# Kernel optimization log

Measured on AMD Instinct MI355X. Metric: run time of the kernel, lower is better.

The kernel has to match this reference:

```python
import jax, jax.numpy as jnp
import numpy as np

B, T, D, H = 512, 2048, 256, 256  # batch, seq_len, input_size, hidden_size


def _uniform(key, shape, fan_in):
    b = 1.0 / np.sqrt(fan_in)
    return jax.random.uniform(key, shape, minval=-b, maxval=b, dtype=jnp.float32)


def setup_inputs() -> dict:
    key = jax.random.key(0)
    ks = jax.random.split(key, 12)
    return {
        "input_tensor": jax.random.normal(ks[0], (B, T, D), dtype=jnp.float32),
        # fc_i: Linear(D, D)
        "Wi": _uniform(ks[1], (D, D), D), "bi": _uniform(ks[2], (D,), D),
        # fc_h: Linear(H, H)
        "Wh": _uniform(ks[3], (H, H), H), "bh": _uniform(ks[4], (H,), H),
        # fc_a: Linear(D, D)
        "Wa": _uniform(ks[5], (D, D), D), "ba": _uniform(ks[6], (D,), D),
        # LSTM(input_size=D, hidden_size=H), gates ordered [i, f, g, o]
        "W_ih": _uniform(ks[7], (4 * H, D), H), "b_ih": _uniform(ks[8], (4 * H,), H),
        "W_hh": _uniform(ks[9], (4 * H, H), H), "b_hh": _uniform(ks[10], (4 * H,), H),
    }


def reference(input_tensor, Wi, bi, Wh, bh, Wa, ba, W_ih, W_hh, b_ih, b_hh):
    x = input_tensor                      # (B, T, D)
    Bb = x.shape[0]
    Hh = Wh.shape[0]
    h0 = jnp.zeros((Bb, Hh), x.dtype)
    c0 = jnp.zeros((Bb, Hh), x.dtype)

    # Per-timestep FC attention; hidden state never updates in the loop,
    # so it vectorizes exactly over T.
    input_o = jnp.einsum('btd,ed->bte', x, Wi) + bi          # (B, T, D)
    hidden_o = h0 @ Wh.T + bh                                # (B, H) == (B, D)
    pre = input_o + hidden_o[:, None, :]                     # (B, T, D)
    attn = jax.nn.sigmoid(jnp.einsum('btd,ed->bte', pre, Wa) + ba)
    attention_output = jnp.sum(attn * x, axis=1)             # (B, D)

    # LSTM over a length-1 sequence (single cell step), PyTorch gate order i,f,g,o
    gates = attention_output @ W_ih.T + b_ih + h0 @ W_hh.T + b_hh
    i, f, g, o = jnp.split(gates, 4, axis=-1)
    i = jax.nn.sigmoid(i); f = jax.nn.sigmoid(f)
    g = jnp.tanh(g); o = jax.nn.sigmoid(o)
    c = f * c0 + i * g
    h = o * jnp.tanh(c)

    lstm_output = h[None]                                    # (1, B, H)
    return (lstm_output, h[None], c[None])
```

## Files before the change

kernel.cpp:

```cpp
#include <hip/hip_runtime.h>
#include <hip/hip_bf16.h>

typedef _Float16 f16x8 __attribute__((ext_vector_type(8)));
typedef _Float16 f16x4 __attribute__((ext_vector_type(4)));
typedef float    f32x4 __attribute__((ext_vector_type(4)));

#define B_SZ 512
#define T_SZ 2048
#define D_SZ 256
#define TCHUNK 16
#define NCHUNK (T_SZ / TCHUNK)

__global__ __launch_bounds__(256) void prep_kernel(
    const float* __restrict__ Wa, const float* __restrict__ Wi,
    const float* __restrict__ bi, const float* __restrict__ bh,
    const float* __restrict__ ba,
    _Float16* __restrict__ Weff, float* __restrict__ beff)
{
    int e = blockIdx.x;
    int d = threadIdx.x;
    float a0 = 0.f, a1 = 0.f, a2 = 0.f, a3 = 0.f;
    #pragma unroll 4
    for (int k = 0; k < 256; k += 4) {
        a0 = fmaf(Wa[e*256 + k    ], Wi[(k    )*256 + d], a0);
        a1 = fmaf(Wa[e*256 + k + 1], Wi[(k + 1)*256 + d], a1);
        a2 = fmaf(Wa[e*256 + k + 2], Wi[(k + 2)*256 + d], a2);
        a3 = fmaf(Wa[e*256 + k + 3], Wi[(k + 3)*256 + d], a3);
    }
    Weff[e*256 + d] = (_Float16)((a0 + a1) + (a2 + a3));

    __shared__ float red[4];
    float s = Wa[e*256 + d] * (bi[d] + bh[d]);
    s += __shfl_down(s, 32, 64);
    s += __shfl_down(s, 16, 64);
    s += __shfl_down(s,  8, 64);
    s += __shfl_down(s,  4, 64);
    s += __shfl_down(s,  2, 64);
    s += __shfl_down(s,  1, 64);
    if ((d & 63) == 0) red[d >> 6] = s;
    __syncthreads();
    if (d == 0) beff[e] = ba[e] + ((red[0] + red[1]) + (red[2] + red[3]));
}

__global__ __launch_bounds__(512, 4) void attn_kernel(
    const float* __restrict__ x,
    const _Float16* __restrict__ Weff,
    const float* __restrict__ beff,
    float* __restrict__ ao)
{
    const int b    = blockIdx.x;
    const int tid  = threadIdx.x;
    const int wave = tid >> 6;
    const int lane = tid & 63;
    const int l15  = lane & 15;
    const int lq   = lane >> 4;

    __shared__ _Float16 xs[2][TCHUNK * 256];
    char* xsb0 = reinterpret_cast<char*>(&xs[0][0]);
    char* xsb1 = reinterpret_cast<char*>(&xs[1][0]);

    const int col0 = wave*32 + l15;
    const int col1 = col0 + 16;
    f16x8 bfA[8], bfB[8];
    #pragma unroll
    for (int ks = 0; ks < 8; ++ks) {
        bfA[ks] = *reinterpret_cast<const f16x8*>(&Weff[col0*256 + ks*32 + lq*8]);
        bfB[ks] = *reinterpret_cast<const f16x8*>(&Weff[col1*256 + ks*32 + lq*8]);
    }
    const f32x4 bcA = *reinterpret_cast<const f32x4*>(&beff[wave*32 + lq*4]);
    const f32x4 bcB = *reinterpret_cast<const f32x4*>(&beff[wave*32 + 16 + lq*4]);

    const float* xb = x + (size_t)b * T_SZ * D_SZ;

    const int srow = tid >> 5;
    const int scg  = tid & 31;
    const float* srcp = xb + (size_t)srow * 256 + scg * 8;
    const int swb = (srow*512 + scg*16) ^ ((srow & 7) << 4);

    #define LOADC(R, c)                                                            \
        {                                                                          \
            const float* p = srcp + (size_t)(c) * (TCHUNK * D_SZ);                 \
            R##0 = *reinterpret_cast<const f32x4*>(p);                             \
            R##1 = *reinterpret_cast<const f32x4*>(p + 4);                         \
        }

    #define WRITE(BUF, R)                                                          \
        {                                                                          \
            f16x8 h;                                                               \
            h[0] = (_Float16)R##0[0]; h[1] = (_Float16)R##0[1];                    \
            h[2] = (_Float16)R##0[2]; h[3] = (_Float16)R##0[3];                    \
            h[4] = (_Float16)R##1[0]; h[5] = (_Float16)R##1[1];                    \
            h[6] = (_Float16)R##1[2]; h[7] = (_Float16)R##1[3];                    \
            *reinterpret_cast<f16x8*>((BUF) + swb) = h;                            \
        }

    #define SYNC()                                                                 \
        {                                                                          \
            asm volatile("s_waitcnt lgkmcnt(0)" ::: "memory");                     \
            __builtin_amdgcn_sched_barrier(0);                                     \
            __builtin_amdgcn_s_barrier();                                          \
        }

    #define COMPUTE(BUF)                                                           \
        {                                                                          \
            const int aswz  = (l15 & 7) << 4;                                      \
            const int abase = l15 * 512;                                           \
            f32x4 acc0 = {0.f, 0.f, 0.f, 0.f};                                     \
            f32x4 acc1 = {0.f, 0.f, 0.f, 0.f};                                     \
            _Pragma("unroll")                                                      \
            for (int ks = 0; ks < 8; ++ks) {                                       \
                int ab = abase + ((ks*64 + lq*16) ^ aswz);                         \
                f16x8 a = *reinterpret_cast<const f16x8*>((BUF) + ab);             \
                acc0 = __builtin_amdgcn_mfma_f32_16x16x32_f16(bfA[ks], a, acc0, 0, 0, 0); \
                acc1 = __builtin_amdgcn_mfma_f32_16x16x32_f16(bfB[ks], a, acc1, 0, 0, 0); \
            }                                                                      \
             \
            int eb0 = abase + (((wave*64      ) + lq*8) ^ aswz);                   \
            int eb1 = abase + (((wave*64 + 32 ) + lq*8) ^ aswz);                   \
            f16x4 xq0 = *reinterpret_cast<const f16x4*>((BUF) + eb0);              \
            f16x4 xq1 = *reinterpret_cast<const f16x4*>((BUF) + eb1);              \
            _Pragma("unroll")                                                      \
            for (int r = 0; r < 4; ++r) {                                          \
                {                                                                  \
                    float s = acc0[r] + bcA[r];                                    \
                    float attn = __builtin_amdgcn_rcpf(1.f + __expf(-s));          \
                    ao0[r] = fmaf(attn, (float)xq0[r], ao0[r]);                    \
                }                                                                  \
                {                                                                  \
                    float s = acc1[r] + bcB[r];                                    \
                    float attn = __builtin_amdgcn_rcpf(1.f + __expf(-s));          \
                    ao1[r] = fmaf(attn, (float)xq1[r], ao1[r]);                    \
                }                                                                  \
            }                                                                      \
        }

    f32x4 ao0 = {0.f, 0.f, 0.f, 0.f};
    f32x4 ao1 = {0.f, 0.f, 0.f, 0.f};
    f32x4 sA0, sA1, sB0, sB1;

    LOADC(sA, 0);
    LOADC(sB, 1);

    for (int c = 0; c < NCHUNK; c += 2) {
        WRITE(xsb0, sA);
        SYNC();
        if (c + 2 < NCHUNK) LOADC(sA, c + 2);
        COMPUTE(xsb0);
        WRITE(xsb1, sB);
        SYNC();
        if (c + 3 < NCHUNK) LOADC(sB, c + 3);
        COMPUTE(xsb1);
    }

    #pragma unroll
    for (int m = 1; m <= 8; m <<= 1) {
        #pragma unroll
        for (int r = 0; r < 4; ++r) {
            ao0[r] += __shfl_xor(ao0[r], m, 64);
            ao1[r] += __shfl_xor(ao1[r], m, 64);
        }
    }
    if (l15 == 0) {
        *reinterpret_cast<f32x4*>(&ao[b*256 + wave*32 +      lq*4]) = ao0;
        *reinterpret_cast<f32x4*>(&ao[b*256 + wave*32 + 16 + lq*4]) = ao1;
    }

    #undef LOADC
    #undef WRITE
    #undef SYNC
    #undef COMPUTE
}

__global__ __launch_bounds__(256) void lstm_kernel(
    const float* __restrict__ ao,
    const float* __restrict__ Wih,
    const float* __restrict__ bih,
    const float* __restrict__ bhh,
    float* __restrict__ out)
{
    int b = blockIdx.x;
    int j = threadIdx.x;
    __shared__ float a[256];
    a[j] = ao[b*256 + j];
    __syncthreads();

    float gi = bih[j]       + bhh[j];
    float gg = bih[512 + j] + bhh[512 + j];
    float go = bih[768 + j] + bhh[768 + j];
    const float* wi = Wih + (size_t)j * 256;
    const float* wg = Wih + (size_t)(512 + j) * 256;
    const float* wo = Wih + (size_t)(768 + j) * 256;
    #pragma unroll 4
    for (int k = 0; k < 256; k += 4) {
        f32x4 w1 = *reinterpret_cast<const f32x4*>(wi + k);
        f32x4 w2 = *reinterpret_cast<const f32x4*>(wg + k);
        f32x4 w3 = *reinterpret_cast<const f32x4*>(wo + k);
        #pragma unroll
        for (int q = 0; q < 4; ++q) {
            float av = a[k + q];
            gi = fmaf(w1[q], av, gi);
            gg = fmaf(w2[q], av, gg);
            go = fmaf(w3[q], av, go);
        }
    }
    float ig = 1.f / (1.f + __expf(-gi));
    float g  = tanhf(gg);
    float og = 1.f / (1.f + __expf(-go));
    float cc = ig * g;
    float hh = og * tanhf(cc);
    out[          b*256 + j] = hh;
    out[131072 +  b*256 + j] = hh;
    out[262144 +  b*256 + j] = cc;
}

extern "C" void kernel_launch(void* const* d_in, const int* in_sizes, int n_in,
                              void* d_out, int out_size, void* d_ws, size_t ws_size,
                              hipStream_t stream) {
    const float* x    = (const float*)d_in[0];
    const float* Wi   = (const float*)d_in[1];
    const float* bi   = (const float*)d_in[2];
    const float* bh   = (const float*)d_in[4];
    const float* Wa   = (const float*)d_in[5];
    const float* ba   = (const float*)d_in[6];
    const float* W_ih = (const float*)d_in[7];
    const float* b_ih = (const float*)d_in[8];
    const float* b_hh = (const float*)d_in[10];

    char* ws = (char*)d_ws;
    _Float16* Weff = (_Float16*)ws;
    float*    beff = (float*)(ws + 128*1024);
    float*    ao   = (float*)(ws + 132*1024);

    prep_kernel<<<256, 256, 0, stream>>>(Wa, Wi, bi, bh, ba, Weff, beff);
    attn_kernel<<<B_SZ, 512, 0, stream>>>(x, Weff, beff, ao);
    lstm_kernel<<<B_SZ, 256, 0, stream>>>(ao, W_ih, b_ih, b_hh, (float*)d_out);
}
```

Measured before the change: 264.4 us.

## Fold sigmoid scaling into weights, reorder chunks, and batch LSTM rows per block

Pre-scales the fused attention weights and bias by -log2(e) so the sigmoid uses exp2 directly, and seeds the MFMA accumulators with the bias. Odd batches walk their time chunks in reverse order, and the next global load is issued before the barrier rather than after it. The LSTM kernel now handles four batch rows per block to reuse each W_ih row load. The f16 weights now carry the scale factor, which could change rounding slightly.

```diff
diff --git a/kernel.cpp b/kernel.cpp
--- a/kernel.cpp
+++ b/kernel.cpp
@@ -17,6 +17,7 @@
     const float* __restrict__ ba,
     _Float16* __restrict__ Weff, float* __restrict__ beff)
 {
+    const float NL2E = -1.4426950408889634f;
     int e = blockIdx.x;
     int d = threadIdx.x;
     float a0 = 0.f, a1 = 0.f, a2 = 0.f, a3 = 0.f;
@@ -27,7 +28,7 @@
         a2 = fmaf(Wa[e*256 + k + 2], Wi[(k + 2)*256 + d], a2);
         a3 = fmaf(Wa[e*256 + k + 3], Wi[(k + 3)*256 + d], a3);
     }
-    Weff[e*256 + d] = (_Float16)((a0 + a1) + (a2 + a3));
+    Weff[e*256 + d] = (_Float16)(NL2E * ((a0 + a1) + (a2 + a3)));
 
     __shared__ float red[4];
     float s = Wa[e*256 + d] * (bi[d] + bh[d]);
@@ -39,7 +40,7 @@
     s += __shfl_down(s,  1, 64);
     if ((d & 63) == 0) red[d >> 6] = s;
     __syncthreads();
-    if (d == 0) beff[e] = ba[e] + ((red[0] + red[1]) + (red[2] + red[3]));
+    if (d == 0) beff[e] = NL2E * (ba[e] + ((red[0] + red[1]) + (red[2] + red[3])));
 }
 
 __global__ __launch_bounds__(512, 4) void attn_kernel(
@@ -72,6 +73,10 @@
 
     const float* xb = x + (size_t)b * T_SZ * D_SZ;
 
+    const int rev   = b & 1;
+    const int cbase = rev ? (NCHUNK - 1) : 0;
+    #define CIDX(c) (rev ? (cbase - (c)) : (c))
+
     const int srow = tid >> 5;
     const int scg  = tid & 31;
     const float* srcp = xb + (size_t)srow * 256 + scg * 8;
@@ -105,8 +110,8 @@
         {                                                                          \
             const int aswz  = (l15 & 7) << 4;                                      \
             const int abase = l15 * 512;                                           \
-            f32x4 acc0 = {0.f, 0.f, 0.f, 0.f};                                     \
-            f32x4 acc1 = {0.f, 0.f, 0.f, 0.f};                                     \
+            f32x4 acc0 = bcA;                                                      \
+            f32x4 acc1 = bcB;                                                      \
             _Pragma("unroll")                                                      \
             for (int ks = 0; ks < 8; ++ks) {                                       \
                 int ab = abase + ((ks*64 + lq*16) ^ aswz);                         \
@@ -114,7 +119,7 @@
                 acc0 = __builtin_amdgcn_mfma_f32_16x16x32_f16(bfA[ks], a, acc0, 0, 0, 0); \
                 acc1 = __builtin_amdgcn_mfma_f32_16x16x32_f16(bfB[ks], a, acc1, 0, 0, 0); \
             }                                                                      \
-             \
+                     \
             int eb0 = abase + (((wave*64      ) + lq*8) ^ aswz);                   \
             int eb1 = abase + (((wave*64 + 32 ) + lq*8) ^ aswz);                   \
             f16x4 xq0 = *reinterpret_cast<const f16x4*>((BUF) + eb0);              \
@@ -122,13 +127,11 @@
             _Pragma("unroll")                                                      \
             for (int r = 0; r < 4; ++r) {                                          \
                 {                                                                  \
-                    float s = acc0[r] + bcA[r];                                    \
-                    float attn = __builtin_amdgcn_rcpf(1.f + __expf(-s));          \
+                    float attn = __builtin_amdgcn_rcpf(1.f + exp2f(acc0[r]));      \
                     ao0[r] = fmaf(attn, (float)xq0[r], ao0[r]);                    \
                 }                                                                  \
                 {                                                                  \
-                    float s = acc1[r] + bcB[r];                                    \
-                    float attn = __builtin_amdgcn_rcpf(1.f + __expf(-s));          \
+                    float attn = __builtin_amdgcn_rcpf(1.f + exp2f(acc1[r]));      \
                     ao1[r] = fmaf(attn, (float)xq1[r], ao1[r]);                    \
                 }                                                                  \
             }                                                                      \
@@ -138,17 +141,17 @@
     f32x4 ao1 = {0.f, 0.f, 0.f, 0.f};
     f32x4 sA0, sA1, sB0, sB1;
 
-    LOADC(sA, 0);
-    LOADC(sB, 1);
+    LOADC(sA, CIDX(0));
+    LOADC(sB, CIDX(1));
 
     for (int c = 0; c < NCHUNK; c += 2) {
         WRITE(xsb0, sA);
+        if (c + 2 < NCHUNK) LOADC(sA, CIDX(c + 2));
         SYNC();
-        if (c + 2 < NCHUNK) LOADC(sA, c + 2);
         COMPUTE(xsb0);
         WRITE(xsb1, sB);
+        if (c + 3 < NCHUNK) LOADC(sB, CIDX(c + 3));
         SYNC();
-        if (c + 3 < NCHUNK) LOADC(sB, c + 3);
         COMPUTE(xsb1);
     }
 
@@ -169,6 +172,7 @@
     #undef WRITE
     #undef SYNC
     #undef COMPUTE
+    #undef CIDX
 }
 
 __global__ __launch_bounds__(256) void lstm_kernel(
@@ -178,39 +182,52 @@
     const float* __restrict__ bhh,
     float* __restrict__ out)
 {
-    int b = blockIdx.x;
-    int j = threadIdx.x;
-    __shared__ float a[256];
-    a[j] = ao[b*256 + j];
+    const int b0 = blockIdx.x * 4;
+    const int j  = threadIdx.x;
+    __shared__ float a[4][256];
+    #pragma unroll
+    for (int bb = 0; bb < 4; ++bb) a[bb][j] = ao[(b0 + bb)*256 + j];
     __syncthreads();
 
-    float gi = bih[j]       + bhh[j];
-    float gg = bih[512 + j] + bhh[512 + j];
-    float go = bih[768 + j] + bhh[768 + j];
+    const float bi_ = bih[j]       + bhh[j];
+    const float bg_ = bih[512 + j] + bhh[512 + j];
+    const float bo_ = bih[768 + j] + bhh[768 + j];
+    float gi[4], gg[4], go[4];
+    #pragma unroll
+    for (int bb = 0; bb < 4; ++bb) { gi[bb] = bi_; gg[bb] = bg_; go[bb] = bo_; }
+
     const float* wi = Wih + (size_t)j * 256;
     const float* wg = Wih + (size_t)(512 + j) * 256;
     const float* wo = Wih + (size_t)(768 + j) * 256;
-    #pragma unroll 4
+    #pragma unroll 2
     for (int k = 0; k < 256; k += 4) {
         f32x4 w1 = *reinterpret_cast<const f32x4*>(wi + k);
         f32x4 w2 = *reinterpret_cast<const f32x4*>(wg + k);
         f32x4 w3 = *reinterpret_cast<const f32x4*>(wo + k);
+        f32x4 av0 = *reinterpret_cast<const f32x4*>(&a[0][k]);
+        f32x4 av1 = *reinterpret_cast<const f32x4*>(&a[1][k]);
+        f32x4 av2 = *reinterpret_cast<const f32x4*>(&a[2][k]);
+        f32x4 av3 = *reinterpret_cast<const f32x4*>(&a[3][k]);
         #pragma unroll
         for (int q = 0; q < 4; ++q) {
-            float av = a[k + q];
-            gi = fmaf(w1[q], av, gi);
-            gg = fmaf(w2[q], av, gg);
-            go = fmaf(w3[q], av, go);
-        }
-    }
-    float ig = 1.f / (1.f + __expf(-gi));
-    float g  = tanhf(gg);
-    float og = 1.f / (1.f + __expf(-go));
-    float cc = ig * g;
-    float hh = og * tanhf(cc);
-    out[          b*256 + j] = hh;
-    out[131072 +  b*256 + j] = hh;
-    out[262144 +  b*256 + j] = cc;
+            gi[0] = fmaf(w1[q], av0[q], gi[0]); gg[0] = fmaf(w2[q], av0[q], gg[0]); go[0] = fmaf(w3[q], av0[q], go[0]);
+            gi[1] = fmaf(w1[q], av1[q], gi[1]); gg[1] = fmaf(w2[q], av1[q], gg[1]); go[1] = fmaf(w3[q], av1[q], go[1]);
+            gi[2] = fmaf(w1[q], av2[q], gi[2]); gg[2] = fmaf(w2[q], av2[q], gg[2]); go[2] = fmaf(w3[q], av2[q], go[2]);
+            gi[3] = fmaf(w1[q], av3[q], gi[3]); gg[3] = fmaf(w2[q], av3[q], gg[3]); go[3] = fmaf(w3[q], av3[q], go[3]);
+        }
+    }
+
+    #pragma unroll
+    for (int bb = 0; bb < 4; ++bb) {
+        float ig = 1.f / (1.f + __expf(-gi[bb]));
+        float g  = tanhf(gg[bb]);
+        float og = 1.f / (1.f + __expf(-go[bb]));
+        float cc = ig * g;
+        float hh = og * tanhf(cc);
+        out[          (b0 + bb)*256 + j] = hh;
+        out[131072 +  (b0 + bb)*256 + j] = hh;
+        out[262144 +  (b0 + bb)*256 + j] = cc;
+    }
 }
 
 extern "C" void kernel_launch(void* const* d_in, const int* in_sizes, int n_in,
@@ -233,5 +250,5 @@
 
     prep_kernel<<<256, 256, 0, stream>>>(Wa, Wi, bi, bh, ba, Weff, beff);
     attn_kernel<<<B_SZ, 512, 0, stream>>>(x, Weff, beff, ao);
-    lstm_kernel<<<B_SZ, 256, 0, stream>>>(ao, W_ih, b_ih, b_hh, (float*)d_out);
-}
+    lstm_kernel<<<128, 256, 0, stream>>>(ao, W_ih, b_ih, b_hh, (float*)d_out);
+}
```

New measurement: 291.4 us. +10.2%, slower.
